# Performance work log

Measured on AMD Instinct MI355X. Metric: run time of the kernel, lower is better.

Reference implementation:

```python
import jax, jax.numpy as jnp
import numpy as np

N_NODES = 50000
N_EDGES = 800000
IN_DIM = 89
HID = 128


def gcn_conv(x, src, dst, deg_inv_sqrt, W, b):
    # PyG GCNConv: x' = D^{-1/2} (A + I) D^{-1/2} (x W) + b
    h = x @ W  # [N, F_out]
    norm = deg_inv_sqrt[src] * deg_inv_sqrt[dst]  # per-edge norm [E]
    msgs = h[src] * norm[:, None]  # gather + scale [E, F_out]
    agg = jax.ops.segment_sum(msgs, dst, num_segments=x.shape[0])
    # self-loop contribution: norm = deg_inv_sqrt[i]^2
    agg = agg + h * (deg_inv_sqrt * deg_inv_sqrt)[:, None]
    return agg + b


def setup_inputs() -> dict:
    key = jax.random.key(0)
    k1, k2, k3, k4, k5, k6 = jax.random.split(key, 6)
    x = jax.random.normal(k1, (N_NODES, IN_DIM), dtype=jnp.float32)
    edge_index = jax.random.randint(k2, (2, N_EDGES), 0, N_NODES, dtype=jnp.int64)
    # Glorot-style init for GCN weights
    W1 = jax.random.normal(k3, (IN_DIM, HID), dtype=jnp.float32) * (1.0 / np.sqrt(IN_DIM))
    b1 = jnp.zeros((HID,), dtype=jnp.float32)
    W2 = jax.random.normal(k4, (HID, HID), dtype=jnp.float32) * (1.0 / np.sqrt(HID))
    b2 = jnp.zeros((HID,), dtype=jnp.float32)
    return {"x": x, "edge_index": edge_index, "W1": W1, "b1": b1, "W2": W2, "b2": b2}


def reference(x, edge_index, W1, b1, W2, b2):
    src = edge_index[0]
    dst = edge_index[1]
    n = x.shape[0]
    # degree of A + I: 1 (self loop) + in-degree
    deg = 1.0 + jax.ops.segment_sum(jnp.ones((src.shape[0],), x.dtype), dst, num_segments=n)
    deg_inv_sqrt = jax.lax.rsqrt(deg)
    h = jax.nn.relu(gcn_conv(x, src, dst, deg_inv_sqrt, W1, b1))
    h = jax.nn.relu(gcn_conv(h, src, dst, deg_inv_sqrt, W2, b2))
    return (h, edge_index)
```

## Files before the change

kernel.cpp:

```cpp
#include <hip/hip_runtime.h>
#include <hip/hip_bf16.h>


#define HID 128
#define KIN 89
#define KP 128
#define BSH 7
#define BNODES 128
#define MAXBUCK 512
#define NPB 128
#define P4CAP 3072

typedef __attribute__((ext_vector_type(8))) short bf16x8;
typedef __attribute__((ext_vector_type(4))) float f32x4;

static __device__ inline float2 unpack_bf16(unsigned v) {
    union { unsigned u; float f; } lo, hi;
    lo.u = v << 16;
    hi.u = v & 0xFFFF0000u;
    return make_float2(lo.f, hi.f);
}

static __device__ inline unsigned pack_bf16(float a, float b) {
    __hip_bfloat162 h = __float22bfloat162_rn(make_float2(a, b));
    return *reinterpret_cast<unsigned*>(&h);
}

static __device__ inline unsigned short f2bf(float v) {
    __hip_bfloat16 h = __float2bfloat16(v);
    return *reinterpret_cast<unsigned short*>(&h);
}

__global__ __launch_bounds__(256) void p1_kernel(
    const int* __restrict__ ei, float* __restrict__ outE,
    int* __restrict__ histG,
    const float* __restrict__ W1, unsigned short* __restrict__ W1t,
    const float* __restrict__ W2, unsigned short* __restrict__ W2t,
    int E, int nbuck)
{
    __shared__ int h[MAXBUCK];
    const int tid = threadIdx.x, blk = blockIdx.x;
    const int* src = ei;
    const int* dst = ei + E;
    for (int b = tid; b < nbuck; b += 256) h[b] = 0;

    int tg = blk * 256 + tid;
    if (tg < HID * KP) {
        int n = tg / KP, k = tg % KP;
        W1t[tg] = f2bf(k < KIN ? W1[(size_t)k * HID + n] : 0.0f);
    } else {
        int t2 = tg - HID * KP;
        if (t2 < HID * HID) {
            int n = t2 / HID, k = t2 % HID;
            W2t[t2] = f2bf(W2[(size_t)k * HID + n]);
        }
    }
    __syncthreads();

    const int chunk = (E + NPB - 1) / NPB;
    const int beg = blk * chunk, end = min(beg + chunk, E);
    for (int i = beg + tid; i < end; i += 256) {
        int d = dst[i];
        atomicAdd(&h[d >> BSH], 1);
        outE[i] = (float)src[i];
        outE[E + i] = (float)d;
    }
    __syncthreads();
    for (int b = tid; b < nbuck; b += 256) histG[b * NPB + blk] = h[b];
}

__global__ __launch_bounds__(NPB) void p2a_kernel(
    int* __restrict__ histG, int* __restrict__ totals)
{
    __shared__ int wsum[NPB / 64];
    const int b = blockIdx.x, tid = threadIdx.x, lane = tid & 63, wid = tid >> 6;
    int c = histG[b * NPB + tid];
    int s = c;
#pragma unroll
    for (int off = 1; off < 64; off <<= 1) {
        int t = __shfl_up(s, off, 64);
        if (lane >= off) s += t;
    }
    if (lane == 63) wsum[wid] = s;
    __syncthreads();
    if (tid == 0) {
        int a = 0;
#pragma unroll
        for (int w = 0; w < NPB / 64; ++w) { int t = wsum[w]; wsum[w] = a; a += t; }
    }
    __syncthreads();
    int excl = wsum[wid] + s - c;
    histG[b * NPB + tid] = excl;
    if (tid == NPB - 1) totals[b] = excl + c;
}

static __device__ inline void scan_totals2(const int* __restrict__ totals,
                                           int* __restrict__ sexcl,
                                           int* __restrict__ wsum,
                                           int nbuck, int tid)
{
    const int lane = tid & 63, wid = tid >> 6;
    const int i0 = 2 * tid, i1 = 2 * tid + 1;
    int t0 = (i0 < nbuck) ? totals[i0] : 0;
    int t1 = (i1 < nbuck) ? totals[i1] : 0;
    int p = t0 + t1;
    int s = p;
#pragma unroll
    for (int off = 1; off < 64; off <<= 1) {
        int t = __shfl_up(s, off, 64);
        if (lane >= off) s += t;
    }
    if (lane == 63) wsum[wid] = s;
    __syncthreads();
    if (tid == 0) {
        int a = 0;
#pragma unroll
        for (int w = 0; w < 4; ++w) { int t = wsum[w]; wsum[w] = a; a += t; }
    }
    __syncthreads();
    int excl = wsum[wid] + s - p;
    sexcl[i0] = excl;
    sexcl[i1] = excl + t0;
}

__global__ __launch_bounds__(256) void p3_part_kernel(
    const int* __restrict__ ei, const int* __restrict__ histG,
    const int* __restrict__ totals, unsigned* __restrict__ ebuf,
    int E, int nbuck)
{
    __shared__ int cur[MAXBUCK];
    __shared__ int wsum[4];
    const int tid = threadIdx.x, blk = blockIdx.x;
    const int* src = ei;
    const int* dst = ei + E;
    scan_totals2(totals, cur, wsum, nbuck, tid);
    __syncthreads();
    for (int b = tid; b < nbuck; b += 256) cur[b] += histG[b * NPB + blk];
    const int chunk = (E + NPB - 1) / NPB;
    const int beg = blk * chunk, end = min(beg + chunk, E);
    __syncthreads();
    for (int i = beg + tid; i < end; i += 256) {
        int d = dst[i];
        int b = d >> BSH;
        int pos = atomicAdd(&cur[b], 1);
        ebuf[pos] = ((unsigned)(d & (BNODES - 1)) << 16) | (unsigned)src[i];
    }
}

__global__ __launch_bounds__(256) void p4_sort_kernel(
    const unsigned* __restrict__ ebuf, const int* __restrict__ totals,
    unsigned short* __restrict__ csr, int* __restrict__ rowptr,
    float* __restrict__ dis, int N, int E, int nbuck)
{
    __shared__ int counts[BNODES];
    __shared__ int cursor[BNODES];
    __shared__ int sbase[MAXBUCK];
    __shared__ int wsum[4];
    __shared__ int w2[2];
    __shared__ unsigned short staging[P4CAP];
    const int b = blockIdx.x, tid = threadIdx.x, lane = tid & 63, wid = tid >> 6;

    scan_totals2(totals, sbase, wsum, nbuck, tid);
    __syncthreads();
    const int gbase = sbase[b];
    const int cnt = totals[b];

    if (tid < BNODES) counts[tid] = 0;
    __syncthreads();
    for (int i = tid; i < cnt; i += 256)
        atomicAdd(&counts[ebuf[gbase + i] >> 16], 1);
    __syncthreads();

    int c = 0, s = 0;
    if (tid < BNODES) {
        c = counts[tid];
        s = c;
#pragma unroll
        for (int off = 1; off < 64; off <<= 1) {
            int t = __shfl_up(s, off, 64);
            if (lane >= off) s += t;
        }
        if (lane == 63) w2[wid] = s;
    }
    __syncthreads();
    if (tid == 0) { int t = w2[0]; w2[0] = 0; w2[1] = t; }
    __syncthreads();
    if (tid < BNODES) {
        int excl = w2[wid] + s - c;
        cursor[tid] = excl;
        int node = b * BNODES + tid;
        if (node < N) {
            rowptr[node] = gbase + excl;
            dis[node] = rsqrtf(1.0f + (float)c);
        }
    }
    if (b == 0 && tid == 0) rowptr[N] = E;
    __syncthreads();

    if (cnt <= P4CAP) {
        for (int i = tid; i < cnt; i += 256) {
            unsigned v = ebuf[gbase + i];
            int pos = atomicAdd(&cursor[v >> 16], 1);
            staging[pos] = (unsigned short)(v & 0xFFFFu);
        }
        __syncthreads();
        for (int i = tid; i < cnt; i += 256)
            csr[gbase + i] = staging[i];
    } else {
        for (int i = tid; i < cnt; i += 256) {
            unsigned v = ebuf[gbase + i];
            int pos = atomicAdd(&cursor[v >> 16], 1);
            csr[gbase + pos] = (unsigned short)(v & 0xFFFFu);
        }
    }
}

__global__ __launch_bounds__(256) void xconv_kernel(
    const float* __restrict__ X, const float* __restrict__ dis,
    unsigned* __restrict__ Xhs, int N)
{
    int t = blockIdx.x * 256 + threadIdx.x;
    if (t >= N * (KP / 2)) return;
    int n = t / (KP / 2), c = t % (KP / 2);
    float d = dis[n];
    const float* xr = X + (size_t)n * KIN;
    float a = (2 * c     < KIN) ? d * xr[2 * c]     : 0.0f;
    float b = (2 * c + 1 < KIN) ? d * xr[2 * c + 1] : 0.0f;
    Xhs[t] = pack_bf16(a, b);
}

__global__ __launch_bounds__(256) void gather_kernel(
    const uint4* __restrict__ rows, const int* __restrict__ rowptr,
    const unsigned short* __restrict__ csr, uint4* __restrict__ aggh, int N)
{
    const int lane = threadIdx.x & 63;
    const int sub  = lane >> 4;
    const int sl   = lane & 15;
    const int node = (blockIdx.x * 4 + (threadIdx.x >> 6)) * 4 + sub;
    const bool valid = node < N;
    const int cn = valid ? node : N - 1;

    uint4 sv = rows[(size_t)cn * 16 + sl];
    float a0, a1, a2, a3, a4, a5, a6, a7;
    {
        float2 p;
        p = unpack_bf16(sv.x); a0 = p.x; a1 = p.y;
        p = unpack_bf16(sv.y); a2 = p.x; a3 = p.y;
        p = unpack_bf16(sv.z); a4 = p.x; a5 = p.y;
        p = unpack_bf16(sv.w); a6 = p.x; a7 = p.y;
    }

    int beg = rowptr[cn];
    int end = valid ? rowptr[cn + 1] : beg;
    int j = beg;
    for (; j + 4 <= end; j += 4) {
        int r0 = csr[j], r1 = csr[j + 1], r2 = csr[j + 2], r3 = csr[j + 3];
        uint4 v0 = rows[(size_t)r0 * 16 + sl];
        uint4 v1 = rows[(size_t)r1 * 16 + sl];
        uint4 v2 = rows[(size_t)r2 * 16 + sl];
        uint4 v3 = rows[(size_t)r3 * 16 + sl];
        float2 p;
        p = unpack_bf16(v0.x); a0 += p.x; a1 += p.y;
        p = unpack_bf16(v0.y); a2 += p.x; a3 += p.y;
        p = unpack_bf16(v0.z); a4 += p.x; a5 += p.y;
        p = unpack_bf16(v0.w); a6 += p.x; a7 += p.y;
        p = unpack_bf16(v1.x); a0 += p.x; a1 += p.y;
        p = unpack_bf16(v1.y); a2 += p.x; a3 += p.y;
        p = unpack_bf16(v1.z); a4 += p.x; a5 += p.y;
        p = unpack_bf16(v1.w); a6 += p.x; a7 += p.y;
        p = unpack_bf16(v2.x); a0 += p.x; a1 += p.y;
        p = unpack_bf16(v2.y); a2 += p.x; a3 += p.y;
        p = unpack_bf16(v2.z); a4 += p.x; a5 += p.y;
        p = unpack_bf16(v2.w); a6 += p.x; a7 += p.y;
        p = unpack_bf16(v3.x); a0 += p.x; a1 += p.y;
        p = unpack_bf16(v3.y); a2 += p.x; a3 += p.y;
        p = unpack_bf16(v3.z); a4 += p.x; a5 += p.y;
        p = unpack_bf16(v3.w); a6 += p.x; a7 += p.y;
    }
    for (; j < end; ++j) {
        int r = csr[j];
        uint4 v = rows[(size_t)r * 16 + sl];
        float2 p;
        p = unpack_bf16(v.x); a0 += p.x; a1 += p.y;
        p = unpack_bf16(v.y); a2 += p.x; a3 += p.y;
        p = unpack_bf16(v.z); a4 += p.x; a5 += p.y;
        p = unpack_bf16(v.w); a6 += p.x; a7 += p.y;
    }

    if (valid)
        aggh[(size_t)node * 16 + sl] =
            make_uint4(pack_bf16(a0, a1), pack_bf16(a2, a3),
                       pack_bf16(a4, a5), pack_bf16(a6, a7));
}

template<int KPA, bool LAYER1>
__global__ __launch_bounds__(256) void mfma_gemm_kernel(
    const unsigned short* __restrict__ A, const unsigned short* __restrict__ Wt,
    const float* __restrict__ bias, const float* __restrict__ dis,
    void* __restrict__ outp, int N)
{
    const int wave = threadIdx.x >> 6;
    const int lane = threadIdx.x & 63;
    const int m    = lane & 15;
    const int quad = lane >> 4;
    const int row0 = blockIdx.x * 64 + wave * 16;
    const int node = row0 + m;

    f32x4 acc[8];
#pragma unroll
    for (int t = 0; t < 8; ++t) acc[t] = (f32x4){0.0f, 0.0f, 0.0f, 0.0f};

    const int arow = min(node, N - 1);
    const unsigned short* arp = A + (size_t)arow * KPA;

#pragma unroll
    for (int c = 0; c < KPA / 32; ++c) {
        const int k0 = c * 32 + quad * 8;
        bf16x8 nv = *(const bf16x8*)(arp + k0);
#pragma unroll
        for (int t = 0; t < 8; ++t) {
            bf16x8 wv = *(const bf16x8*)(Wt + (size_t)(t * 16 + m) * KPA + k0);
            acc[t] = __builtin_amdgcn_mfma_f32_16x16x32_bf16(wv, nv, acc[t], 0, 0, 0);
        }
    }

    if (node < N) {
        const float dv = dis[node];
#pragma unroll
        for (int t = 0; t < 8; ++t) {
            const int col0 = t * 16 + quad * 4;
            float4 bb = *(const float4*)&bias[col0];
            float r0 = fmaxf(fmaf(dv, acc[t][0], bb.x), 0.0f);
            float r1 = fmaxf(fmaf(dv, acc[t][1], bb.y), 0.0f);
            float r2 = fmaxf(fmaf(dv, acc[t][2], bb.z), 0.0f);
            float r3 = fmaxf(fmaf(dv, acc[t][3], bb.w), 0.0f);
            if (LAYER1) {
                uint2 u;
                u.x = pack_bf16(r0 * dv, r1 * dv);
                u.y = pack_bf16(r2 * dv, r3 * dv);
                *(uint2*)((unsigned short*)outp + (size_t)node * HID + col0) = u;
            } else {
                float4 r = make_float4(r0, r1, r2, r3);
                *(float4*)((float*)outp + (size_t)node * HID + col0) = r;
            }
        }
    }
}


static inline char* wsal(char*& p, size_t n) {
    uintptr_t q = ((uintptr_t)p + 255) & ~(uintptr_t)255;
    char* r = (char*)q;
    p = r + n;
    return r;
}

extern "C" void kernel_launch(void* const* d_in, const int* in_sizes, int n_in,
                              void* d_out, int out_size, void* d_ws, size_t ws_size,
                              hipStream_t stream) {
    const float* x  = (const float*)d_in[0];
    const int*   ei = (const int*)d_in[1];
    const float* W1 = (const float*)d_in[2];
    const float* b1 = (const float*)d_in[3];
    const float* W2 = (const float*)d_in[4];
    const float* b2 = (const float*)d_in[5];

    const int N = in_sizes[0] / KIN;
    const int E = in_sizes[1] / 2;
    const int nbuck = (N + BNODES - 1) >> BSH;

    float* out  = (float*)d_out;
    float* outH = out;
    float* outE = out + (size_t)N * HID;

    char* ws = (char*)d_ws;
    int*            histG  = (int*)wsal(ws, (size_t)MAXBUCK * NPB * 4);
    int*            totals = (int*)wsal(ws, MAXBUCK * 4);
    int*            rowptr = (int*)wsal(ws, (size_t)(N + 1) * 4);
    float*          dis    = (float*)wsal(ws, (size_t)N * 4);
    unsigned*       ebuf   = (unsigned*)wsal(ws, (size_t)E * 4);
    unsigned short* csr    = (unsigned short*)wsal(ws, (size_t)E * 2);
    unsigned*       Xhs    = (unsigned*)wsal(ws, (size_t)N * (KP / 2) * 4);
    unsigned*       agg1h  = (unsigned*)wsal(ws, (size_t)N * (KP / 2) * 4);
    unsigned short* g2h    = (unsigned short*)wsal(ws, (size_t)N * HID * 2);
    unsigned short* agg2h  = (unsigned short*)wsal(ws, (size_t)N * HID * 2);
    unsigned short* W1t    = (unsigned short*)wsal(ws, (size_t)HID * KP * 2);
    unsigned short* W2t    = (unsigned short*)wsal(ws, (size_t)HID * HID * 2);

    p1_kernel<<<NPB, 256, 0, stream>>>(ei, outE, histG, W1, W1t, W2, W2t, E, nbuck);
    p2a_kernel<<<nbuck, NPB, 0, stream>>>(histG, totals);
    p3_part_kernel<<<NPB, 256, 0, stream>>>(ei, histG, totals, ebuf, E, nbuck);
    p4_sort_kernel<<<nbuck, 256, 0, stream>>>(ebuf, totals, csr, rowptr, dis,
                                              N, E, nbuck);
    xconv_kernel<<<(N * (KP / 2) + 255) / 256, 256, 0, stream>>>(x, dis, Xhs, N);

    const int ngt = (N + 15) / 16;
    const int ngm = (N + 63) / 64;

    gather_kernel<<<ngt, 256, 0, stream>>>((const uint4*)Xhs, rowptr, csr,
                                           (uint4*)agg1h, N);
    mfma_gemm_kernel<KP, true><<<ngm, 256, 0, stream>>>(
        (const unsigned short*)agg1h, W1t, b1, dis, g2h, N);

    gather_kernel<<<ngt, 256, 0, stream>>>((const uint4*)g2h, rowptr, csr,
                                           (uint4*)agg2h, N);
    mfma_gemm_kernel<HID, false><<<ngm, 256, 0, stream>>>(
        agg2h, W2t, b2, dis, outH, N);
}
```

Before: 226.7 us.

## Fuse neighbor gather with MFMA GEMM through LDS staging per layer

```diff
diff --git a/kernel.cpp b/kernel.cpp
--- a/kernel.cpp
+++ b/kernel.cpp
@@ -10,6 +10,7 @@
 #define MAXBUCK 512
 #define NPB 128
 #define P4CAP 3072
+#define LDSPAD 136
 
 typedef __attribute__((ext_vector_type(8))) short bf16x8;
 typedef __attribute__((ext_vector_type(4))) float f32x4;
@@ -229,97 +230,98 @@
     Xhs[t] = pack_bf16(a, b);
 }
 
-__global__ __launch_bounds__(256) void gather_kernel(
+template<bool LAYER1>
+__global__ __launch_bounds__(256) void fused_kernel(
     const uint4* __restrict__ rows, const int* __restrict__ rowptr,
-    const unsigned short* __restrict__ csr, uint4* __restrict__ aggh, int N)
-{
-    const int lane = threadIdx.x & 63;
-    const int sub  = lane >> 4;
+    const unsigned short* __restrict__ csr,
+    const unsigned short* __restrict__ Wt, const float* __restrict__ bias,
+    const float* __restrict__ dis, void* __restrict__ outp, int N)
+{
+    __shared__ unsigned short lds_a[64][LDSPAD];
+    const int tid  = threadIdx.x;
+    const int wave = tid >> 6;
+    const int lane = tid & 63;
+    const int sub  = (lane >> 4) & 3;
     const int sl   = lane & 15;
-    const int node = (blockIdx.x * 4 + (threadIdx.x >> 6)) * 4 + sub;
-    const bool valid = node < N;
-    const int cn = valid ? node : N - 1;
-
-    uint4 sv = rows[(size_t)cn * 16 + sl];
-    float a0, a1, a2, a3, a4, a5, a6, a7;
-    {
-        float2 p;
-        p = unpack_bf16(sv.x); a0 = p.x; a1 = p.y;
-        p = unpack_bf16(sv.y); a2 = p.x; a3 = p.y;
-        p = unpack_bf16(sv.z); a4 = p.x; a5 = p.y;
-        p = unpack_bf16(sv.w); a6 = p.x; a7 = p.y;
-    }
-
-    int beg = rowptr[cn];
-    int end = valid ? rowptr[cn + 1] : beg;
-    int j = beg;
-    for (; j + 4 <= end; j += 4) {
-        int r0 = csr[j], r1 = csr[j + 1], r2 = csr[j + 2], r3 = csr[j + 3];
-        uint4 v0 = rows[(size_t)r0 * 16 + sl];
-        uint4 v1 = rows[(size_t)r1 * 16 + sl];
-        uint4 v2 = rows[(size_t)r2 * 16 + sl];
-        uint4 v3 = rows[(size_t)r3 * 16 + sl];
-        float2 p;
-        p = unpack_bf16(v0.x); a0 += p.x; a1 += p.y;
-        p = unpack_bf16(v0.y); a2 += p.x; a3 += p.y;
-        p = unpack_bf16(v0.z); a4 += p.x; a5 += p.y;
-        p = unpack_bf16(v0.w); a6 += p.x; a7 += p.y;
-        p = unpack_bf16(v1.x); a0 += p.x; a1 += p.y;
-        p = unpack_bf16(v1.y); a2 += p.x; a3 += p.y;
-        p = unpack_bf16(v1.z); a4 += p.x; a5 += p.y;
-        p = unpack_bf16(v1.w); a6 += p.x; a7 += p.y;
-        p = unpack_bf16(v2.x); a0 += p.x; a1 += p.y;
-        p = unpack_bf16(v2.y); a2 += p.x; a3 += p.y;
-        p = unpack_bf16(v2.z); a4 += p.x; a5 += p.y;
-        p = unpack_bf16(v2.w); a6 += p.x; a7 += p.y;
-        p = unpack_bf16(v3.x); a0 += p.x; a1 += p.y;
-        p = unpack_bf16(v3.y); a2 += p.x; a3 += p.y;
-        p = unpack_bf16(v3.z); a4 += p.x; a5 += p.y;
-        p = unpack_bf16(v3.w); a6 += p.x; a7 += p.y;
-    }
-    for (; j < end; ++j) {
-        int r = csr[j];
-        uint4 v = rows[(size_t)r * 16 + sl];
-        float2 p;
-        p = unpack_bf16(v.x); a0 += p.x; a1 += p.y;
-        p = unpack_bf16(v.y); a2 += p.x; a3 += p.y;
-        p = unpack_bf16(v.z); a4 += p.x; a5 += p.y;
-        p = unpack_bf16(v.w); a6 += p.x; a7 += p.y;
-    }
-
-    if (valid)
-        aggh[(size_t)node * 16 + sl] =
-            make_uint4(pack_bf16(a0, a1), pack_bf16(a2, a3),
-                       pack_bf16(a4, a5), pack_bf16(a6, a7));
-}
-
-template<int KPA, bool LAYER1>
-__global__ __launch_bounds__(256) void mfma_gemm_kernel(
-    const unsigned short* __restrict__ A, const unsigned short* __restrict__ Wt,
-    const float* __restrict__ bias, const float* __restrict__ dis,
-    void* __restrict__ outp, int N)
-{
-    const int wave = threadIdx.x >> 6;
-    const int lane = threadIdx.x & 63;
+    const int blk0 = blockIdx.x * 64;
+
+#pragma unroll
+    for (int p = 0; p < 4; ++p) {
+        const int lrow = wave * 16 + p * 4 + sub;
+        const int node = blk0 + lrow;
+        const bool valid = node < N;
+        const int cn = valid ? node : N - 1;
+
+        uint4 sv = rows[(size_t)cn * 16 + sl];
+        float a0, a1, a2, a3, a4, a5, a6, a7;
+        {
+            float2 q;
+            q = unpack_bf16(sv.x); a0 = q.x; a1 = q.y;
+            q = unpack_bf16(sv.y); a2 = q.x; a3 = q.y;
+            q = unpack_bf16(sv.z); a4 = q.x; a5 = q.y;
+            q = unpack_bf16(sv.w); a6 = q.x; a7 = q.y;
+        }
+
+        int beg = rowptr[cn];
+        int end = valid ? rowptr[cn + 1] : beg;
+        int j = beg;
+        for (; j + 4 <= end; j += 4) {
+            int r0 = csr[j], r1 = csr[j + 1], r2 = csr[j + 2], r3 = csr[j + 3];
+            uint4 v0 = rows[(size_t)r0 * 16 + sl];
+            uint4 v1 = rows[(size_t)r1 * 16 + sl];
+            uint4 v2 = rows[(size_t)r2 * 16 + sl];
+            uint4 v3 = rows[(size_t)r3 * 16 + sl];
+            float2 q;
+            q = unpack_bf16(v0.x); a0 += q.x; a1 += q.y;
+            q = unpack_bf16(v0.y); a2 += q.x; a3 += q.y;
+            q = unpack_bf16(v0.z); a4 += q.x; a5 += q.y;
+            q = unpack_bf16(v0.w); a6 += q.x; a7 += q.y;
+            q = unpack_bf16(v1.x); a0 += q.x; a1 += q.y;
+            q = unpack_bf16(v1.y); a2 += q.x; a3 += q.y;
+            q = unpack_bf16(v1.z); a4 += q.x; a5 += q.y;
+            q = unpack_bf16(v1.w); a6 += q.x; a7 += q.y;
+            q = unpack_bf16(v2.x); a0 += q.x; a1 += q.y;
+            q = unpack_bf16(v2.y); a2 += q.x; a3 += q.y;
+            q = unpack_bf16(v2.z); a4 += q.x; a5 += q.y;
+            q = unpack_bf16(v2.w); a6 += q.x; a7 += q.y;
+            q = unpack_bf16(v3.x); a0 += q.x; a1 += q.y;
+            q = unpack_bf16(v3.y); a2 += q.x; a3 += q.y;
+            q = unpack_bf16(v3.z); a4 += q.x; a5 += q.y;
+            q = unpack_bf16(v3.w); a6 += q.x; a7 += q.y;
+        }
+        for (; j < end; ++j) {
+            int r = csr[j];
+            uint4 v = rows[(size_t)r * 16 + sl];
+            float2 q;
+            q = unpack_bf16(v.x); a0 += q.x; a1 += q.y;
+            q = unpack_bf16(v.y); a2 += q.x; a3 += q.y;
+            q = unpack_bf16(v.z); a4 += q.x; a5 += q.y;
+            q = unpack_bf16(v.w); a6 += q.x; a7 += q.y;
+        }
+
+        uint4 pk = make_uint4(pack_bf16(a0, a1), pack_bf16(a2, a3),
+                              pack_bf16(a4, a5), pack_bf16(a6, a7));
+        *(uint4*)&lds_a[lrow][sl * 8] = pk;
+    }
+    __syncthreads();
+
     const int m    = lane & 15;
     const int quad = lane >> 4;
-    const int row0 = blockIdx.x * 64 + wave * 16;
-    const int node = row0 + m;
+    const int node = blk0 + wave * 16 + m;
 
     f32x4 acc[8];
 #pragma unroll
     for (int t = 0; t < 8; ++t) acc[t] = (f32x4){0.0f, 0.0f, 0.0f, 0.0f};
 
-    const int arow = min(node, N - 1);
-    const unsigned short* arp = A + (size_t)arow * KPA;
-
-#pragma unroll
-    for (int c = 0; c < KPA / 32; ++c) {
+    const unsigned short* arp = &lds_a[wave * 16 + m][0];
+
+#pragma unroll
+    for (int c = 0; c < KP / 32; ++c) {
         const int k0 = c * 32 + quad * 8;
         bf16x8 nv = *(const bf16x8*)(arp + k0);
 #pragma unroll
         for (int t = 0; t < 8; ++t) {
-            bf16x8 wv = *(const bf16x8*)(Wt + (size_t)(t * 16 + m) * KPA + k0);
+            bf16x8 wv = *(const bf16x8*)(Wt + (size_t)(t * 16 + m) * KP + k0);
             acc[t] = __builtin_amdgcn_mfma_f32_16x16x32_bf16(wv, nv, acc[t], 0, 0, 0);
         }
     }
@@ -381,9 +383,7 @@
     unsigned*       ebuf   = (unsigned*)wsal(ws, (size_t)E * 4);
     unsigned short* csr    = (unsigned short*)wsal(ws, (size_t)E * 2);
     unsigned*       Xhs    = (unsigned*)wsal(ws, (size_t)N * (KP / 2) * 4);
-    unsigned*       agg1h  = (unsigned*)wsal(ws, (size_t)N * (KP / 2) * 4);
     unsigned short* g2h    = (unsigned short*)wsal(ws, (size_t)N * HID * 2);
-    unsigned short* agg2h  = (unsigned short*)wsal(ws, (size_t)N * HID * 2);
     unsigned short* W1t    = (unsigned short*)wsal(ws, (size_t)HID * KP * 2);
     unsigned short* W2t    = (unsigned short*)wsal(ws, (size_t)HID * HID * 2);
 
@@ -394,16 +394,11 @@
                                               N, E, nbuck);
     xconv_kernel<<<(N * (KP / 2) + 255) / 256, 256, 0, stream>>>(x, dis, Xhs, N);
 
-    const int ngt = (N + 15) / 16;
-    const int ngm = (N + 63) / 64;
-
-    gather_kernel<<<ngt, 256, 0, stream>>>((const uint4*)Xhs, rowptr, csr,
-                                           (uint4*)agg1h, N);
-    mfma_gemm_kernel<KP, true><<<ngm, 256, 0, stream>>>(
-        (const unsigned short*)agg1h, W1t, b1, dis, g2h, N);
-
-    gather_kernel<<<ngt, 256, 0, stream>>>((const uint4*)g2h, rowptr, csr,
-                                           (uint4*)agg2h, N);
-    mfma_gemm_kernel<HID, false><<<ngm, 256, 0, stream>>>(
-        agg2h, W2t, b2, dis, outH, N);
-}
+    const int ngf = (N + 63) / 64;
+
+    fused_kernel<true><<<ngf, 256, 0, stream>>>(
+        (const uint4*)Xhs, rowptr, csr, W1t, b1, dis, g2h, N);
+
+    fused_kernel<false><<<ngf, 256, 0, stream>>>(
+        (const uint4*)g2h, rowptr, csr, W2t, b2, dis, outH, N);
+}
```

New measurement: 220.7 us. 1.03x faster.
